# Optimization experiments

Measured on AMD Instinct MI355X. Metric: run time of the kernel, lower is better.

## Reference

```python
import jax, jax.numpy as jnp
import numpy as np

SEQ = 110          # input_size1 = sample_width*2
HALF = SEQ // 2    # 55
N_EMBD = 102       # n_chrom + 2
HEAD = 192

def _cross_half_mask():
    # attention allowed only between the two halves (same-half blocks masked)
    idx = jnp.arange(SEQ)
    same_half = (idx[:, None] < HALF) == (idx[None, :] < HALF)
    return same_half  # True where attention is DISALLOWED

def setup_inputs() -> dict:
    key = jax.random.key(0)
    k1, k2, k3, k4 = jax.random.split(key, 4)
    B = 8192
    x = jax.random.normal(k1, (B, SEQ, N_EMBD), dtype=jnp.float32)
    Wq = jax.random.normal(k2, (N_EMBD, HEAD), dtype=jnp.float32) * (N_EMBD ** -0.5)
    Wk = jax.random.normal(k3, (N_EMBD, HEAD), dtype=jnp.float32) * (N_EMBD ** -0.5)
    Wv = jax.random.normal(k4, (N_EMBD, HEAD), dtype=jnp.float32) * (N_EMBD ** -0.5)
    return {"x": x, "Wq": Wq, "Wk": Wk, "Wv": Wv}

def reference(x, Wq, Wk, Wv):
    # q,k,v: [B, S, H]
    q = x @ Wq
    k = x @ Wk
    v = x @ Wv
    scale = HEAD ** -0.5
    scores = jnp.einsum('bsh,bth->bst', q, k) * scale  # [B, S, S]
    mask = _cross_half_mask()                           # [S, S] True = masked
    scores = jnp.where(mask, -jnp.inf, scores)
    attn = jax.nn.softmax(scores, axis=-1)
    # dropout is identity at inference (p=0.15 at train)
    out = jnp.einsum('bst,bth->bsh', attn, v)           # [B, S, H]
    return out
```

## Files before the change

kernel.cpp:

```cpp
#include <hip/hip_runtime.h>
#include <hip/hip_bf16.h>

#define SEQ   110
#define HALFS 55
#define EMB   102
#define HEAD  192

typedef short bf16x8 __attribute__((ext_vector_type(8)));
typedef float f32x4  __attribute__((ext_vector_type(4)));

#define XS    104
#define XTILE (64 * XS)
#define MTS   128
#define MTROWS 112
#define MT_SHORTS (MTROWS * MTS)
#define WES   128

__device__ __forceinline__ short f2bf(float f) {
    unsigned u = __float_as_uint(f);
    unsigned r = u + 0x7fffu + ((u >> 16) & 1u);
    return (short)(r >> 16);
}
__device__ __forceinline__ unsigned pk2(float a, float b) {
    return ((unsigned)(unsigned short)f2bf(b) << 16) | (unsigned short)f2bf(a);
}

__global__ void prep(const float* __restrict__ Wq, const float* __restrict__ Wk,
                     const float* __restrict__ Wv, short* __restrict__ ws) {
    int flat = blockIdx.x * 256 + threadIdx.x;
    if (flat < MT_SHORTS) {
        int i = flat >> 7, j = flat & 127;
        float v = 0.0f;
        if (i < EMB && j < EMB) {
            const float4* q4 = (const float4*)(Wq + j * HEAD);
            const float4* k4 = (const float4*)(Wk + i * HEAD);
            float s = 0.0f;
            #pragma unroll 4
            for (int h4 = 0; h4 < HEAD / 4; ++h4) {
                float4 a = q4[h4], b = k4[h4];
                s += a.x * b.x + a.y * b.y + a.z * b.z + a.w * b.w;
            }
            v = s * 0.07216878364870322f;
        }
        ws[flat] = f2bf(v);
    } else if (flat < MT_SHORTS + HEAD * WES) {
        int idx = flat - MT_SHORTS;
        int h = idx >> 7, e = idx & 127;
        float v = (e < EMB) ? Wv[e * HEAD + h] : 0.0f;
        ws[flat] = f2bf(v);
    }
}

__global__ __launch_bounds__(256, 2)
void attn_head(const float* __restrict__ x, const short* __restrict__ ws,
               float* __restrict__ out, int B) {
    const int tid  = threadIdx.x;
    const int w    = tid >> 6;
    const int lane = tid & 63;
    const int g    = lane >> 4;
    const int r    = lane & 15;

    __shared__ __attribute__((aligned(16))) short u[3 * XTILE];
    short* slotA = u;
    short* slotB = u + XTILE;
    short* slotC = u + 2 * XTILE;

    const short* Mt  = ws;
    const short* WvT = ws + MT_SHORTS;

    bf16x8 wvf[3][4];
    #pragma unroll
    for (int mi = 0; mi < 3; ++mi) {
        const int hrow = 16 * (w + 4 * mi) + r;
        #pragma unroll
        for (int kk = 0; kk < 4; ++kk)
            wvf[mi][kk] = *(const bf16x8*)(WvT + hrow * WES + 32 * kk + 8 * g);
    }

    {
        unsigned long long* z = (unsigned long long*)u;
        #pragma unroll
        for (int i0 = 0; i0 < 2; ++i0) {
            int ii = tid + i0 * 256;
            if (ii < 468) z[(ii < 234 ? 1430 : 2860) + ii] = 0ull;
        }
        if (tid < 110)
            *(unsigned*)(u + (tid & 1) * XTILE + (tid >> 1) * XS + 102) = 0u;
    }

    unsigned xv0[11], xv1[11];
    auto loadx = [&](int batch) {
        const float4* xb4 = (const float4*)(x + (size_t)batch * (SEQ * EMB));
        #pragma unroll
        for (int it = 0; it < 11; ++it) {
            int i4 = tid + it * 256;
            if (i4 < 2805) { float4 v = xb4[i4]; xv0[it] = pk2(v.x, v.y); xv1[it] = pk2(v.z, v.w); }
        }
    };
    auto stagex = [&]() {
        #pragma unroll
        for (int it = 0; it < 11; ++it) {
            int i4 = tid + it * 256;
            if (i4 < 2805) {
                int fc  = i4 * 4;
                int row = (int)(((unsigned long long)fc * 41121ull) >> 22);
                int e   = fc - row * EMB;
                int tile = row >= HALFS;
                int lr   = row - HALFS * tile;
                int ba   = tile * XTILE + lr * XS + e;
                if (e == 100) {
                    int rowb  = row + 1;
                    int tileb = rowb >= HALFS;
                    int lrb   = rowb - HALFS * tileb;
                    *(unsigned*)(u + ba) = xv0[it];
                    *(unsigned*)(u + tileb * XTILE + lrb * XS) = xv1[it];
                } else {
                    uint2 t2; t2.x = xv0[it]; t2.y = xv1[it];
                    *(uint2*)(u + ba) = t2;
                }
            }
        }
    };

    loadx(blockIdx.x);
    const int stride = (int)gridDim.x;

    bf16x8 ax[4][4];
    bf16x8 zz = {};

    #pragma unroll 1
    for (int p = blockIdx.x; p < B; p += stride) {
        stagex();
        __syncthreads();

        bf16x8 am[2][4];
        #pragma unroll
        for (int mi2 = 0; mi2 < 2; ++mi2) {
            const int mt = w + 4 * mi2;
            #pragma unroll
            for (int kk = 0; kk < 4; ++kk)
                am[mi2][kk] = (mt < 7) ? *(const bf16x8*)(Mt + (16 * mt + r) * MTS + 32 * kk + 8 * g) : zz;
        }

        #pragma unroll
        for (int stl = 0; stl < 4; ++stl) {
            const short* xb = slotA + (16 * stl + r) * XS;
            bf16x8 bx[4];
            #pragma unroll
            for (int kk = 0; kk < 3; ++kk) bx[kk] = *(const bf16x8*)(xb + 32 * kk + 8 * g);
            bx[3] = zz;
            if (g == 0) bx[3] = *(const bf16x8*)(xb + 96);
            #pragma unroll
            for (int mi2 = 0; mi2 < 2; ++mi2) {
                const int mt = w + 4 * mi2;
                if (mt < 7) {
                    f32x4 acc = {0.f, 0.f, 0.f, 0.f};
                    #pragma unroll
                    for (int kk = 0; kk < 4; ++kk)
                        acc = __builtin_amdgcn_mfma_f32_16x16x32_bf16(am[mi2][kk], bx[kk], acc, 0, 0, 0);
                    if (mt < 6 || g < 2) {
                        uint2 t2; t2.x = pk2(acc[0], acc[1]); t2.y = pk2(acc[2], acc[3]);
                        *(uint2*)(slotC + (16 * stl + r) * XS + 16 * mt + 4 * g) = t2;
                    }
                }
            }
        }
        __syncthreads();

        #pragma unroll
        for (int mt = 0; mt < 4; ++mt) {
            const short* xb = slotB + (16 * mt + r) * XS;
            #pragma unroll
            for (int kk = 0; kk < 3; ++kk) ax[mt][kk] = *(const bf16x8*)(xb + 32 * kk + 8 * g);
            ax[mt][3] = zz;
            if (g == 0) ax[mt][3] = *(const bf16x8*)(xb + 96);
        }
        __syncthreads();

        #pragma unroll
        for (int stl = 0; stl < 4; ++stl) {
            #pragma unroll
            for (int mi2 = 0; mi2 < 2; ++mi2) {
                const int mt = w + 4 * mi2;
                if (mt < 7) {
                    f32x4 acc = {0.f, 0.f, 0.f, 0.f};
                    #pragma unroll
                    for (int kk = 0; kk < 4; ++kk)
                        acc = __builtin_amdgcn_mfma_f32_16x16x32_bf16(am[mi2][kk], ax[stl][kk], acc, 0, 0, 0);
                    if (mt < 6 || g < 2) {
                        uint2 t2; t2.x = pk2(acc[0], acc[1]); t2.y = pk2(acc[2], acc[3]);
                        *(uint2*)(slotB + (16 * stl + r) * XS + 16 * mt + 4 * g) = t2;
                    }
                }
            }
        }

        if (p + stride < B) loadx(p + stride);

        const int src0 = ((g & 1) << 5) + r;
        const int src1 = src0 + 16;
        const bool hi  = (g >> 1) != 0;

        #pragma unroll 1
        for (int half = 0; half < 2; ++half) {
            if (half == 1) {
                __syncthreads();
                #pragma unroll
                for (int mt = 0; mt < 4; ++mt) {
                    const short* xb = slotA + (16 * mt + r) * XS;
                    #pragma unroll
                    for (int kk = 0; kk < 3; ++kk) ax[mt][kk] = *(const bf16x8*)(xb + 32 * kk + 8 * g);
                    ax[mt][3] = zz;
                    if (g == 0) ax[mt][3] = *(const bf16x8*)(xb + 96);
                }
            }
            const short* yo = half ? slotB : slotC;

            unsigned vpk[4][3][2];
            #pragma unroll
            for (int st = 0; st < 4; ++st) {
                #pragma unroll
                for (int mi = 0; mi < 3; ++mi) {
                    f32x4 acc = {0.f, 0.f, 0.f, 0.f};
                    #pragma unroll
                    for (int kk = 0; kk < 4; ++kk)
                        acc = __builtin_amdgcn_mfma_f32_16x16x32_bf16(ax[st][kk], wvf[mi][kk], acc, 0, 0, 0);
                    vpk[st][mi][0] = pk2(acc[0], acc[1]);
                    vpk[st][mi][1] = pk2(acc[2], acc[3]);
                }
            }

            bf16x8 va[3][2];
            #pragma unroll
            for (int mi = 0; mi < 3; ++mi) {
                unsigned e00 = (unsigned)__shfl((int)vpk[0][mi][0], src0), e01 = (unsigned)__shfl((int)vpk[0][mi][1], src0);
                unsigned e02 = (unsigned)__shfl((int)vpk[0][mi][0], src1), e03 = (unsigned)__shfl((int)vpk[0][mi][1], src1);
                unsigned f00 = (unsigned)__shfl((int)vpk[1][mi][0], src0), f01 = (unsigned)__shfl((int)vpk[1][mi][1], src0);
                unsigned f02 = (unsigned)__shfl((int)vpk[1][mi][0], src1), f03 = (unsigned)__shfl((int)vpk[1][mi][1], src1);
                uint4 u0;
                u0.x = hi ? f00 : e00; u0.y = hi ? f01 : e01; u0.z = hi ? f02 : e02; u0.w = hi ? f03 : e03;
                unsigned e10 = (unsigned)__shfl((int)vpk[2][mi][0], src0), e11 = (unsigned)__shfl((int)vpk[2][mi][1], src0);
                unsigned e12 = (unsigned)__shfl((int)vpk[2][mi][0], src1), e13 = (unsigned)__shfl((int)vpk[2][mi][1], src1);
                unsigned f10 = (unsigned)__shfl((int)vpk[3][mi][0], src0), f11 = (unsigned)__shfl((int)vpk[3][mi][1], src0);
                unsigned f12 = (unsigned)__shfl((int)vpk[3][mi][0], src1), f13 = (unsigned)__shfl((int)vpk[3][mi][1], src1);
                uint4 u1;
                u1.x = hi ? f10 : e10; u1.y = hi ? f11 : e11; u1.z = hi ? f12 : e12; u1.w = hi ? f13 : e13;
                __builtin_memcpy(&va[mi][0], &u0, 16);
                __builtin_memcpy(&va[mi][1], &u1, 16);
            }

            const size_t obase = (size_t)p * (SEQ * HEAD) + (size_t)(half * HALFS) * HEAD;

            #pragma unroll 1
            for (int c = 0; c < 4; ++c) {
                const short* yb = yo + (16 * c + r) * XS;
                bf16x8 by[4];
                #pragma unroll
                for (int kk = 0; kk < 3; ++kk) by[kk] = *(const bf16x8*)(yb + 32 * kk + 8 * g);
                by[3] = zz;
                if (g == 0) by[3] = *(const bf16x8*)(yb + 96);

                float sc[4][4];
                #pragma unroll
                for (int mt = 0; mt < 4; ++mt) {
                    f32x4 acc = {0.f, 0.f, 0.f, 0.f};
                    #pragma unroll
                    for (int kk = 0; kk < 4; ++kk)
                        acc = __builtin_amdgcn_mfma_f32_16x16x32_bf16(ax[mt][kk], by[kk], acc, 0, 0, 0);
                    #pragma unroll
                    for (int j = 0; j < 4; ++j) sc[mt][j] = acc[j];
                }
                #pragma unroll
                for (int j = 0; j < 4; ++j)
                    if (48 + 4 * g + j >= HALFS) sc[3][j] = -1e30f;

                float mx = -1e30f;
                #pragma unroll
                for (int mt = 0; mt < 4; ++mt) {
                    #pragma unroll
                    for (int j = 0; j < 4; ++j) mx = fmaxf(mx, sc[mt][j]);
                }
                mx = fmaxf(mx, __shfl_xor(mx, 16));
                mx = fmaxf(mx, __shfl_xor(mx, 32));
                float pr[4][4];
                float sum = 0.f;
                #pragma unroll
                for (int mt = 0; mt < 4; ++mt) {
                    #pragma unroll
                    for (int j = 0; j < 4; ++j) { pr[mt][j] = __expf(sc[mt][j] - mx); sum += pr[mt][j]; }
                }
                sum += __shfl_xor(sum, 16);
                sum += __shfl_xor(sum, 32);
                float rs = 1.0f / sum;

                unsigned pu[4][2];
                #pragma unroll
                for (int mt = 0; mt < 4; ++mt) {
                    pu[mt][0] = pk2(pr[mt][0] * rs, pr[mt][1] * rs);
                    pu[mt][1] = pk2(pr[mt][2] * rs, pr[mt][3] * rs);
                }
                unsigned A00 = (unsigned)__shfl((int)pu[0][0], src0), A01 = (unsigned)__shfl((int)pu[0][1], src0);
                unsigned A02 = (unsigned)__shfl((int)pu[0][0], src1), A03 = (unsigned)__shfl((int)pu[0][1], src1);
                unsigned B00 = (unsigned)__shfl((int)pu[1][0], src0), B01 = (unsigned)__shfl((int)pu[1][1], src0);
                unsigned B02 = (unsigned)__shfl((int)pu[1][0], src1), B03 = (unsigned)__shfl((int)pu[1][1], src1);
                unsigned C00 = (unsigned)__shfl((int)pu[2][0], src0), C01 = (unsigned)__shfl((int)pu[2][1], src0);
                unsigned C02 = (unsigned)__shfl((int)pu[2][0], src1), C03 = (unsigned)__shfl((int)pu[2][1], src1);
                unsigned D00 = (unsigned)__shfl((int)pu[3][0], src0), D01 = (unsigned)__shfl((int)pu[3][1], src0);
                unsigned D02 = (unsigned)__shfl((int)pu[3][0], src1), D03 = (unsigned)__shfl((int)pu[3][1], src1);
                uint4 q0, q1;
                q0.x = hi ? B00 : A00; q0.y = hi ? B01 : A01; q0.z = hi ? B02 : A02; q0.w = hi ? B03 : A03;
                q1.x = hi ? D00 : C00; q1.y = hi ? D01 : C01; q1.z = hi ? D02 : C02; q1.w = hi ? D03 : C03;
                bf16x8 bp0, bp1;
                __builtin_memcpy(&bp0, &q0, 16);
                __builtin_memcpy(&bp1, &q1, 16);

                const int srow  = 16 * c + r;
                const bool valid = srow < HALFS;
                float* orow = out + obase + (size_t)srow * HEAD;
                #pragma unroll
                for (int mi = 0; mi < 3; ++mi) {
                    f32x4 acc = {0.f, 0.f, 0.f, 0.f};
                    acc = __builtin_amdgcn_mfma_f32_16x16x32_bf16(va[mi][0], bp0, acc, 0, 0, 0);
                    acc = __builtin_amdgcn_mfma_f32_16x16x32_bf16(va[mi][1], bp1, acc, 0, 0, 0);
                    if (valid) {
                        float4 st4; st4.x = acc[0]; st4.y = acc[1]; st4.z = acc[2]; st4.w = acc[3];
                        *(float4*)(orow + 16 * (w + 4 * mi) + 4 * g) = st4;
                    }
                }
            }
        }
        __syncthreads();
    }
}

extern "C" void kernel_launch(void* const* d_in, const int* in_sizes, int n_in,
                              void* d_out, int out_size, void* d_ws, size_t ws_size,
                              hipStream_t stream) {
    const float* x  = (const float*)d_in[0];
    const float* Wq = (const float*)d_in[1];
    const float* Wk = (const float*)d_in[2];
    const float* Wv = (const float*)d_in[3];
    short* ws = (short*)d_ws;
    int B = in_sizes[0] / (SEQ * EMB);
    int prep_elems = MT_SHORTS + HEAD * WES;
    prep<<<(prep_elems + 255) / 256, 256, 0, stream>>>(Wq, Wk, Wv, ws);
    attn_head<<<512, 256, 0, stream>>>(x, ws, (float*)d_out, B);
}
```

Before: 354.0 us.

## Split score/softmax rows across waves and share probabilities via LDS

```diff
diff --git a/kernel.cpp b/kernel.cpp
--- a/kernel.cpp
+++ b/kernel.cpp
@@ -11,6 +11,7 @@
 
 #define XS    104
 #define XTILE (64 * XS)
+#define PS    72
 #define MTS   128
 #define MTROWS 112
 #define MT_SHORTS (MTROWS * MTS)
@@ -61,6 +62,7 @@
     const int r    = lane & 15;
 
     __shared__ __attribute__((aligned(16))) short u[3 * XTILE];
+    __shared__ __attribute__((aligned(16))) short P_lds[64 * PS];
     short* slotA = u;
     short* slotB = u + XTILE;
     short* slotC = u + 2 * XTILE;
@@ -249,11 +251,8 @@
                 __builtin_memcpy(&va[mi][1], &u1, 16);
             }
 
-            const size_t obase = (size_t)p * (SEQ * HEAD) + (size_t)(half * HALFS) * HEAD;
-
-            #pragma unroll 1
-            for (int c = 0; c < 4; ++c) {
-                const short* yb = yo + (16 * c + r) * XS;
+            {
+                const short* yb = yo + (16 * w + r) * XS;
                 bf16x8 by[4];
                 #pragma unroll
                 for (int kk = 0; kk < 3; ++kk) by[kk] = *(const bf16x8*)(yb + 32 * kk + 8 * g);
@@ -293,27 +292,22 @@
                 sum += __shfl_xor(sum, 32);
                 float rs = 1.0f / sum;
 
-                unsigned pu[4][2];
-                #pragma unroll
-                for (int mt = 0; mt < 4; ++mt) {
-                    pu[mt][0] = pk2(pr[mt][0] * rs, pr[mt][1] * rs);
-                    pu[mt][1] = pk2(pr[mt][2] * rs, pr[mt][3] * rs);
-                }
-                unsigned A00 = (unsigned)__shfl((int)pu[0][0], src0), A01 = (unsigned)__shfl((int)pu[0][1], src0);
-                unsigned A02 = (unsigned)__shfl((int)pu[0][0], src1), A03 = (unsigned)__shfl((int)pu[0][1], src1);
-                unsigned B00 = (unsigned)__shfl((int)pu[1][0], src0), B01 = (unsigned)__shfl((int)pu[1][1], src0);
-                unsigned B02 = (unsigned)__shfl((int)pu[1][0], src1), B03 = (unsigned)__shfl((int)pu[1][1], src1);
-                unsigned C00 = (unsigned)__shfl((int)pu[2][0], src0), C01 = (unsigned)__shfl((int)pu[2][1], src0);
-                unsigned C02 = (unsigned)__shfl((int)pu[2][0], src1), C03 = (unsigned)__shfl((int)pu[2][1], src1);
-                unsigned D00 = (unsigned)__shfl((int)pu[3][0], src0), D01 = (unsigned)__shfl((int)pu[3][1], src0);
-                unsigned D02 = (unsigned)__shfl((int)pu[3][0], src1), D03 = (unsigned)__shfl((int)pu[3][1], src1);
-                uint4 q0, q1;
-                q0.x = hi ? B00 : A00; q0.y = hi ? B01 : A01; q0.z = hi ? B02 : A02; q0.w = hi ? B03 : A03;
-                q1.x = hi ? D00 : C00; q1.y = hi ? D01 : C01; q1.z = hi ? D02 : C02; q1.w = hi ? D03 : C03;
-                bf16x8 bp0, bp1;
-                __builtin_memcpy(&bp0, &q0, 16);
-                __builtin_memcpy(&bp1, &q1, 16);
-
+                #pragma unroll
+                for (int mt = 0; mt < 4; ++mt) {
+                    uint2 t2;
+                    t2.x = pk2(pr[mt][0] * rs, pr[mt][1] * rs);
+                    t2.y = pk2(pr[mt][2] * rs, pr[mt][3] * rs);
+                    *(uint2*)(P_lds + (16 * w + r) * PS + 16 * mt + 4 * g) = t2;
+                }
+            }
+            __syncthreads();
+
+            const size_t obase = (size_t)p * (SEQ * HEAD) + (size_t)(half * HALFS) * HEAD;
+            #pragma unroll
+            for (int c = 0; c < 4; ++c) {
+                const short* pb = P_lds + (16 * c + r) * PS + 8 * g;
+                bf16x8 bp0 = *(const bf16x8*)(pb);
+                bf16x8 bp1 = *(const bf16x8*)(pb + 32);
                 const int srow  = 16 * c + r;
                 const bool valid = srow < HALFS;
                 float* orow = out + obase + (size_t)srow * HEAD;
```

Result: faster. 336.3 us (-5.0%).
